# Kernel tuning notes

Measured on AMD Instinct MI355X. Metric: run time of the kernel, lower is better.

## Reference

```python
import jax, jax.numpy as jnp
import numpy as np

EPS = 1e-5  # torch BatchNorm2d default eps (eval mode with running stats)


def bn(x, g, b, m, v):
    # x: [B,C,H,W]; per-channel affine batchnorm in inference form
    return (x - m[:, None, None]) * (g[:, None, None] / jnp.sqrt(v[:, None, None] + EPS)) + b[:, None, None]


def self_attn(x, Wq, bq, Wk, bk, Wv, bv, rel_h, rel_w):
    # x: [B,C,H,W]; Wq/Wk/Wv: [C,C] (1x1 convs); rel_h: [C,H]; rel_w: [C,W]
    B, C, H, W = x.shape
    N = H * W
    q = jnp.einsum('oc,bchw->bohw', Wq, x).reshape(B, C, N) + bq[None, :, None]
    k = jnp.einsum('oc,bchw->bohw', Wk, x).reshape(B, C, N) + bk[None, :, None]
    v = jnp.einsum('oc,bchw->bohw', Wv, x).reshape(B, C, N) + bv[None, :, None]
    energy = jnp.einsum('bcn,bcm->bnm', q, k)                      # content: Q^T K
    pos = (rel_h[:, :, None] + rel_w[:, None, :]).reshape(C, N)    # [C, H*W]
    energy = energy + jnp.einsum('bcn,cm->bnm', q, pos)            # rel-pos bias term
    attn = jax.nn.softmax(energy, axis=-1)                         # [B,N,N]
    out = jnp.einsum('bcm,bnm->bcn', v, attn)                      # V @ attn^T
    return out.reshape(B, C, H, W)


def conv3x3(x, w):
    return jax.lax.conv_general_dilated(x, w, (1, 1), 'SAME',
                                        dimension_numbers=('NCHW', 'OIHW', 'NCHW'))


def setup_inputs() -> dict:
    key = jax.random.key(0)
    B, C, H, W, NH = 32, 512, 16, 16, 5
    ks = jax.random.split(key, 32)
    f = lambda i, shape, s=1.0: jax.random.normal(ks[i], shape, jnp.float32) * s
    inp = {
        'x0': f(0, (B, C, H, W)), 'x1': f(1, (B, C, H, W)), 'x2': f(2, (B, C, H, W)),
        'x3': f(3, (B, C, H, W)), 'x': f(4, (B, C, H, W)),
        'qW': f(5, (NH, C, C), 0.02), 'qB': f(6, (NH, C), 0.02),
        'kW': f(7, (NH, C, C), 0.02), 'kB': f(8, (NH, C), 0.02),
        'vW': f(9, (NH, C, C), 0.02), 'vB': f(10, (NH, C), 0.02),
        'relH': f(11, (NH, C, H)), 'relW': f(12, (NH, C, W)),
        'msw_W': f(13, (NH - 1, NH * C), 0.02),
        'msw_g': jnp.ones((NH - 1,)), 'msw_b': jnp.zeros((NH - 1,)),
        'msw_m': jnp.zeros((NH - 1,)), 'msw_v': jnp.ones((NH - 1,)),
        'fus_W': f(14, (C, C, 3, 3), 0.02),
        'fus_g': jnp.ones((C,)), 'fus_b': jnp.zeros((C,)),
        'fus_m': jnp.zeros((C,)), 'fus_v': jnp.ones((C,)),
        'top_g': jnp.ones((C,)), 'top_b': jnp.zeros((C,)),
        'top_m': jnp.zeros((C,)), 'top_v': jnp.ones((C,)),
        'h': 16, 'w': 16,
    }
    return inp


def reference(x0, x1, x2, x3, x, qW, qB, kW, kB, vW, vB, relH, relW,
              msw_W, msw_g, msw_b, msw_m, msw_v,
              fus_W, fus_g, fus_b, fus_m, fus_v,
              top_g, top_b, top_m, top_v, h, w):
    B, C, H, W = x.shape
    xs = jnp.stack([x0, x1, x2, x3, x])                            # [5,B,C,H,W]
    outs = jax.vmap(self_attn)(xs, qW, qB, kW, kB, vW, vB, relH, relW)  # [5,B,C,H,W]
    cat = outs.transpose(1, 0, 2, 3, 4).reshape(B, 5 * C, H, W)
    weights = jax.nn.sigmoid(bn(jnp.einsum('oc,bchw->bohw', msw_W, cat),
                                msw_g, msw_b, msw_m, msw_v))        # [B,4,H,W]
    x_ms = (weights[:, 0:1] * outs[0] + weights[:, 1:2] * outs[1]
            + weights[:, 2:3] * outs[2] + weights[:, 3:4] * outs[3] + outs[4])
    x_ms = jax.nn.relu(bn(conv3x3(x_ms, fus_W), fus_g, fus_b, fus_m, fus_v))
    out = jax.nn.relu(bn(x_ms + x, top_g, top_b, top_m, top_v))
    return out
```

## Files before the change

### kernel.cpp

```cpp
#include <hip/hip_runtime.h>
#include <cstdint>

using bf16x8  = __attribute__((ext_vector_type(8))) __bf16;
using f32x4   = __attribute__((ext_vector_type(4))) float;
using ushort8 = __attribute__((ext_vector_type(8))) unsigned short;

#define EPSN 1e-5f

__device__ __forceinline__ void gld16(const void* g, void* l) {
  __builtin_amdgcn_global_load_lds((const __attribute__((address_space(1))) void*)g,
                                   (__attribute__((address_space(3))) void*)l, 16, 0, 0);
}

__device__ __forceinline__ ushort f2bf(float f) {
  union { float f; uint32_t u; } v; v.f = f;
  uint32_t r = v.u + 0x7fffu + ((v.u >> 16) & 1u);
  return (ushort)(r >> 16);
}
__device__ __forceinline__ float bf2f(ushort u) {
  union { uint32_t u; float f; } v; v.u = ((uint32_t)u) << 16; return v.f;
}

__device__ __forceinline__ void gemm_core(const ushort* __restrict__ Ag,
                                          const ushort* __restrict__ Bg,
                                          int ldk, int ksteps,
                                          ushort* As, ushort* Bs,
                                          f32x4 (&acc)[4][4]) {
  const int t = threadIdx.x, lane = t & 63, w = t >> 6;
  const int wr = w >> 1, wc = w & 1;
  for (int kt = 0; kt < ksteps; ++kt) {
    const int kbase = kt * 64;
#pragma unroll
    for (int p = 0; p < 4; ++p) {
      int q = p * 256 + t;
      int row = q >> 3, slot = q & 7;
      int srcs = slot ^ (row & 7);
      gld16(Ag + (size_t)row * ldk + kbase + srcs * 8, As + (p * 256 + w * 64) * 8);
      gld16(Bg + (size_t)row * ldk + kbase + srcs * 8, Bs + (p * 256 + w * 64) * 8);
    }
    __syncthreads();
#pragma unroll
    for (int kk = 0; kk < 2; ++kk) {
      bf16x8 af[4], bfv[4];
#pragma unroll
      for (int i = 0; i < 4; ++i) {
        int ra = wr * 64 + i * 16 + (lane & 15);
        int sa = (kk * 4 + (lane >> 4)) ^ (ra & 7);
        af[i] = *(const bf16x8*)(As + ra * 64 + sa * 8);
        int rb = wc * 64 + i * 16 + (lane & 15);
        int sb = (kk * 4 + (lane >> 4)) ^ (rb & 7);
        bfv[i] = *(const bf16x8*)(Bs + rb * 64 + sb * 8);
      }
#pragma unroll
      for (int i = 0; i < 4; ++i)
#pragma unroll
        for (int j = 0; j < 4; ++j)
          acc[i][j] = __builtin_amdgcn_mfma_f32_16x16x32_bf16(af[i], bfv[j], acc[i][j], 0, 0, 0);
    }
    __syncthreads();
  }
}

__global__ __launch_bounds__(256) void k_cvtW(const float* __restrict__ qW,
                                              const float* __restrict__ kW,
                                              const float* __restrict__ vW,
                                              ushort* __restrict__ Wb) {
  int idx = blockIdx.x * 256 + threadIdx.x;
  int gi = idx * 4;
  int sel = gi / 1310720;
  int off = gi - sel * 1310720;
  const float* src = sel == 0 ? qW : (sel == 1 ? kW : vW);
  float4 vv = *(const float4*)(src + off);
  int h = off / 262144, rest = off - h * 262144;
  ushort4 o;
  o.x = f2bf(vv.x); o.y = f2bf(vv.y); o.z = f2bf(vv.z); o.w = f2bf(vv.w);
  *(ushort4*)(Wb + (size_t)(h * 3 + sel) * 262144 + rest) = o;
}

__global__ __launch_bounds__(256) void k_cvtWconv(const float* __restrict__ fusW,
                                                  ushort* __restrict__ Wconv) {
  int p = blockIdx.x * 256 + threadIdx.x;
  const float* src = fusW + (size_t)p * 9;
  float vv[9];
#pragma unroll
  for (int s = 0; s < 9; ++s) vv[s] = src[s];
#pragma unroll
  for (int s = 0; s < 9; ++s) Wconv[(size_t)s * 262144 + p] = f2bf(vv[s]);
}

__global__ __launch_bounds__(256) void k_pos(const float* __restrict__ relH,
                                             const float* __restrict__ relW,
                                             ushort* __restrict__ posb) {
  int idx = blockIdx.x * 256 + threadIdx.x;
  int c = idx & 511, m = (idx >> 9) & 255, h = idx >> 17;
  posb[idx] = f2bf(relH[((size_t)h * 512 + c) * 16 + (m >> 4)] +
                   relW[((size_t)h * 512 + c) * 16 + (m & 15)]);
}

__global__ __launch_bounds__(256) void k_transx(const float* __restrict__ x0,
                                                const float* __restrict__ x1,
                                                const float* __restrict__ x2,
                                                const float* __restrict__ x3,
                                                const float* __restrict__ x4,
                                                ushort* __restrict__ xT) {
  int bid = blockIdx.x;
  const int nt4 = bid & 3;  bid >>= 2;
  const int ct  = bid & 7;  bid >>= 3;
  const int b   = bid & 31; bid >>= 5;
  const int ix  = bid;
  const float* xs = ix == 0 ? x0 : ix == 1 ? x1 : ix == 2 ? x2 : ix == 3 ? x3 : x4;
  const float* src = xs + ((size_t)b * 512 + ct * 64) * 256 + nt4 * 64;
  __shared__ float tile[64][65];
  const int t = threadIdx.x;
  const int col = t & 63, rq = t >> 6;
#pragma unroll
  for (int rr = 0; rr < 16; ++rr) {
    int row = rr * 4 + rq;
    tile[row][col] = src[(size_t)row * 256 + col];
  }
  __syncthreads();
  ushort* dst = xT + ((size_t)(ix * 32 + b) * 256 + nt4 * 64) * 512 + ct * 64;
#pragma unroll
  for (int rr = 0; rr < 16; ++rr) {
    int nrow = rr * 4 + rq;
    dst[(size_t)nrow * 512 + col] = f2bf(tile[col][nrow]);
  }
}

__global__ __launch_bounds__(256) void k_qkv(const ushort* __restrict__ Wb,
                                             const ushort* __restrict__ xT,
                                             const ushort* __restrict__ posb,
                                             const float* __restrict__ qB,
                                             const float* __restrict__ kB,
                                             const float* __restrict__ vB,
                                             ushort* __restrict__ qT,
                                             ushort* __restrict__ kpT,
                                             ushort* __restrict__ vv) {
  __shared__ ushort lds[128 * 144];
  ushort* As = lds;
  ushort* Bs = lds + 8192;
  int bid = blockIdx.x;
  bid = (bid & 7) * 480 + (bid >> 3);
  const int h = bid / 768;
  const int r = bid % 768;
  const int t = threadIdx.x, lane = t & 63, w = t >> 6;
  const int wr = w >> 1, wc = w & 1, g = lane >> 4, l = lane & 15;

  f32x4 acc[4][4];
#pragma unroll
  for (int i = 0; i < 4; ++i)
#pragma unroll
    for (int j = 0; j < 4; ++j) acc[i][j] = f32x4{0.f, 0.f, 0.f, 0.f};

  if (r < 512) {
    const int pt = r >> 3, ot = r & 7;
    const bool isq = ot < 4;
    const ushort* Ag = xT + ((size_t)h * 8192 + pt * 128) * 512;
    const ushort* Bg = Wb + ((size_t)(h * 3 + (isq ? 0 : 1)) * 512 + (ot & 3) * 128) * 512;
    gemm_core(Ag, Bg, 512, 8, As, Bs, acc);

    const float* bias = (isq ? qB : kB) + h * 512 + (ot & 3) * 128;
    float bj[4];
#pragma unroll
    for (int j = 0; j < 4; ++j) bj[j] = bias[wc * 64 + j * 16 + l];
    ushort(*Cs)[144] = (ushort(*)[144])lds;
#pragma unroll
    for (int i = 0; i < 4; ++i)
#pragma unroll
      for (int j = 0; j < 4; ++j)
#pragma unroll
        for (int rr = 0; rr < 4; ++rr)
          Cs[wr * 64 + i * 16 + g * 4 + rr][wc * 64 + j * 16 + l] = f2bf(acc[i][j][rr] + bj[j]);
    __syncthreads();
    ushort* dst = isq ? qT : kpT;
#pragma unroll
    for (int it = 0; it < 8; ++it) {
      int lin = it * 256 + t;
      int row = lin >> 4, cc = (lin & 15) * 8;
      int pglob = pt * 128 + row;
      ushort8 cv = *(const ushort8*)&Cs[row][cc];
      if (!isq) {
        ushort8 pv = *(const ushort8*)(posb + ((size_t)h * 256 + (pglob & 255)) * 512 +
                                       (ot & 3) * 128 + cc);
#pragma unroll
        for (int e = 0; e < 8; ++e) cv[e] = f2bf(bf2f(cv[e]) + bf2f(pv[e]));
      }
      *(ushort8*)(dst + ((size_t)h * 8192 + pglob) * 512 + (ot & 3) * 128 + cc) = cv;
    }
  } else {
    const int r2 = r - 512;
    const int mt = r2 >> 6, ntp = r2 & 63;
    const ushort* Ag = Wb + ((size_t)(h * 3 + 2) * 512 + mt * 128) * 512;
    const ushort* Bg = xT + ((size_t)h * 8192 + ntp * 128) * 512;
    gemm_core(Ag, Bg, 512, 8, As, Bs, acc);

    const float* biasv = vB + h * 512 + mt * 128;
    ushort(*Cs)[144] = (ushort(*)[144])lds;
#pragma unroll
    for (int i = 0; i < 4; ++i)
#pragma unroll
      for (int rr = 0; rr < 4; ++rr) {
        int oloc = wr * 64 + i * 16 + g * 4 + rr;
        float bv = biasv[oloc];
#pragma unroll
        for (int j = 0; j < 4; ++j)
          Cs[oloc][wc * 64 + j * 16 + l] = f2bf(acc[i][j][rr] + bv);
      }
    __syncthreads();
    const int b = ntp >> 1, nb = (ntp & 1) * 128;
#pragma unroll
    for (int it = 0; it < 8; ++it) {
      int lin = it * 256 + t;
      int row = lin >> 4, cc = (lin & 15) * 8;
      ushort8 cv = *(const ushort8*)&Cs[row][cc];
      *(ushort8*)(vv + (((size_t)(h * 32 + b)) * 512 + mt * 128 + row) * 256 + nb + cc) = cv;
    }
  }
}

__global__ __launch_bounds__(256) void k_attn(const ushort* __restrict__ qT,
                                              const ushort* __restrict__ kpT,
                                              ushort* __restrict__ attn) {
  __shared__ ushort As[64 * 64];
  __shared__ ushort Bs[256 * 64];
  __shared__ float red[4][64];
  __shared__ float comb[64];
  int bid = blockIdx.x;
  bid = (bid & 7) * 80 + (bid >> 3);
  const int rt = bid & 3;
  const int hb = bid >> 2;
  const ushort* Ag = qT + ((size_t)hb * 256 + rt * 64) * 512;
  const ushort* Bg = kpT + (size_t)hb * 256 * 512;
  const int t = threadIdx.x, lane = t & 63, w = t >> 6, g = lane >> 4, l = lane & 15;

  f32x4 acc[4][4];
#pragma unroll
  for (int i = 0; i < 4; ++i)
#pragma unroll
    for (int j = 0; j < 4; ++j) acc[i][j] = f32x4{0.f, 0.f, 0.f, 0.f};

  for (int kt = 0; kt < 8; ++kt) {
    const int kbase = kt * 64;
#pragma unroll
    for (int p = 0; p < 2; ++p) {
      int q = p * 256 + t;
      int row = q >> 3, slot = q & 7, srcs = slot ^ (row & 7);
      gld16(Ag + (size_t)row * 512 + kbase + srcs * 8, As + (p * 256 + w * 64) * 8);
    }
#pragma unroll
    for (int p = 0; p < 8; ++p) {
      int q = p * 256 + t;
      int row = q >> 3, slot = q & 7, srcs = slot ^ (row & 7);
      gld16(Bg + (size_t)row * 512 + kbase + srcs * 8, Bs + (p * 256 + w * 64) * 8);
    }
    __syncthreads();
#pragma unroll
    for (int kk = 0; kk < 2; ++kk) {
      bf16x8 af[4], bfv[4];
#pragma unroll
      for (int i = 0; i < 4; ++i) {
        int ra = i * 16 + l;
        int sa = (kk * 4 + g) ^ (ra & 7);
        af[i] = *(const bf16x8*)(As + ra * 64 + sa * 8);
        int rb = w * 64 + i * 16 + l;
        int sb = (kk * 4 + g) ^ (rb & 7);
        bfv[i] = *(const bf16x8*)(Bs + rb * 64 + sb * 8);
      }
#pragma unroll
      for (int i = 0; i < 4; ++i)
#pragma unroll
        for (int j = 0; j < 4; ++j)
          acc[i][j] = __builtin_amdgcn_mfma_f32_16x16x32_bf16(af[i], bfv[j], acc[i][j], 0, 0, 0);
    }
    __syncthreads();
  }

#pragma unroll
  for (int i = 0; i < 4; ++i)
#pragma unroll
    for (int rr = 0; rr < 4; ++rr) {
      float v = fmaxf(fmaxf(acc[i][0][rr], acc[i][1][rr]), fmaxf(acc[i][2][rr], acc[i][3][rr]));
#pragma unroll
      for (int m = 1; m < 16; m <<= 1) v = fmaxf(v, __shfl_xor(v, m));
      if (l == 0) red[w][i * 16 + g * 4 + rr] = v;
    }
  __syncthreads();
  if (t < 64) comb[t] = fmaxf(fmaxf(red[0][t], red[1][t]), fmaxf(red[2][t], red[3][t]));
  __syncthreads();
#pragma unroll
  for (int i = 0; i < 4; ++i)
#pragma unroll
    for (int rr = 0; rr < 4; ++rr) {
      float mx = comb[i * 16 + g * 4 + rr];
      float s = 0.f;
#pragma unroll
      for (int j = 0; j < 4; ++j) {
        float e = expf(acc[i][j][rr] - mx);
        acc[i][j][rr] = e;
        s += e;
      }
#pragma unroll
      for (int m = 1; m < 16; m <<= 1) s += __shfl_xor(s, m);
      if (l == 0) red[w][i * 16 + g * 4 + rr] = s;
    }
  __syncthreads();
  if (t < 64) comb[t] = red[0][t] + red[1][t] + red[2][t] + red[3][t];
  __syncthreads();
  ushort* Arow = attn + (size_t)hb * 65536 + (size_t)rt * 64 * 256;
#pragma unroll
  for (int i = 0; i < 4; ++i)
#pragma unroll
    for (int rr = 0; rr < 4; ++rr) {
      int row = i * 16 + g * 4 + rr;
      float inv = 1.f / comb[row];
#pragma unroll
      for (int j = 0; j < 4; ++j)
        Arow[(size_t)row * 256 + w * 64 + j * 16 + l] = f2bf(acc[i][j][rr] * inv);
    }
}

__global__ __launch_bounds__(256) void k_pv(const ushort* __restrict__ attn,
                                            const ushort* __restrict__ vv,
                                            ushort* __restrict__ OT) {
  __shared__ ushort lds[128 * 144];
  ushort* As = lds;
  ushort* Bs = lds + 8192;
  int bid = blockIdx.x;
  bid = (bid & 7) * 160 + (bid >> 3);
  const int nt = bid & 3; bid >>= 2;
  const int mt = bid & 1; bid >>= 1;
  const size_t hb = (size_t)bid;
  const ushort* Ag = attn + (hb * 256 + mt * 128) * 256;
  const ushort* Bg = vv + (hb * 512 + nt * 128) * 256;
  f32x4 acc[4][4];
#pragma unroll
  for (int i = 0; i < 4; ++i)
#pragma unroll
    for (int j = 0; j < 4; ++j) acc[i][j] = f32x4{0.f, 0.f, 0.f, 0.f};
  gemm_core(Ag, Bg, 256, 4, As, Bs, acc);
  const int t = threadIdx.x, lane = t & 63, w = t >> 6;
  const int wr = w >> 1, wc = w & 1, g = lane >> 4, l = lane & 15;
  ushort(*Cs)[144] = (ushort(*)[144])lds;
#pragma unroll
  for (int i = 0; i < 4; ++i)
#pragma unroll
    for (int j = 0; j < 4; ++j)
#pragma unroll
      for (int rr = 0; rr < 4; ++rr)
        Cs[wr * 64 + i * 16 + g * 4 + rr][wc * 64 + j * 16 + l] = f2bf(acc[i][j][rr]);
  __syncthreads();
#pragma unroll
  for (int it = 0; it < 8; ++it) {
    int lin = it * 256 + t;
    int row = lin >> 4, cc = (lin & 15) * 8;
    ushort8 cv = *(const ushort8*)&Cs[row][cc];
    *(ushort8*)(OT + (hb * 256 + mt * 128 + row) * 512 + nt * 128 + cc) = cv;
  }
}

__global__ __launch_bounds__(256) void k_weights(const ushort* __restrict__ OT,
                                                 const float* __restrict__ mswW,
                                                 const float* __restrict__ mg,
                                                 const float* __restrict__ mb,
                                                 const float* __restrict__ mm,
                                                 const float* __restrict__ mv,
                                                 ushort* __restrict__ xmsT) {
  __shared__ float Os[2560];
  __shared__ float part[4][4];
  __shared__ float wsh[4];
  const int t = threadIdx.x, lane = t & 63, w = t >> 6;
  const size_t pix = blockIdx.x;
  for (int h = 0; h < 5; ++h)
    for (int c = t; c < 512; c += 256)
      Os[h * 512 + c] = bf2f(OT[((size_t)h * 8192 + pix) * 512 + c]);
  __syncthreads();
  float a0 = 0.f, a1 = 0.f, a2 = 0.f, a3 = 0.f;
  for (int i = t; i < 2560; i += 256) {
    float o = Os[i];
    a0 += mswW[i] * o;
    a1 += mswW[2560 + i] * o;
    a2 += mswW[5120 + i] * o;
    a3 += mswW[7680 + i] * o;
  }
#pragma unroll
  for (int m = 1; m < 64; m <<= 1) {
    a0 += __shfl_xor(a0, m); a1 += __shfl_xor(a1, m);
    a2 += __shfl_xor(a2, m); a3 += __shfl_xor(a3, m);
  }
  if (lane == 0) { part[w][0] = a0; part[w][1] = a1; part[w][2] = a2; part[w][3] = a3; }
  __syncthreads();
  if (t < 4) {
    float dot = part[0][t] + part[1][t] + part[2][t] + part[3][t];
    float val = (dot - mm[t]) * (mg[t] * rsqrtf(mv[t] + EPSN)) + mb[t];
    wsh[t] = 1.f / (1.f + expf(-val));
  }
  __syncthreads();
  for (int c = t; c < 512; c += 256) {
    float val = wsh[0] * Os[c] + wsh[1] * Os[512 + c] + wsh[2] * Os[1024 + c] +
                wsh[3] * Os[1536 + c] + Os[2048 + c];
    xmsT[pix * 512 + c] = f2bf(val);
  }
}

__global__ __launch_bounds__(256) void k_conv(const ushort* __restrict__ Wconv,
                                              const ushort* __restrict__ xmsT,
                                              float* __restrict__ y1a,
                                              float* __restrict__ y1b) {
  __shared__ ushort As[128 * 64];
  __shared__ ushort xp[180 * 72];
  int bid = blockIdx.x;
  bid = (bid & 7) * 64 + (bid >> 3);
  const int ntl = bid & 1; bid >>= 1;
  const int mt = bid & 3;  bid >>= 2;
  const int halfk = bid & 1; bid >>= 1;
  const int bb = bid;
  const int y0 = ntl * 8;
  const int t = threadIdx.x, lane = t & 63, w = t >> 6, wr = w >> 1, wc = w & 1;
  f32x4 acc[4][4];
#pragma unroll
  for (int i = 0; i < 4; ++i)
#pragma unroll
    for (int j = 0; j < 4; ++j) acc[i][j] = f32x4{0.f, 0.f, 0.f, 0.f};

  for (int cb = halfk * 4; cb < halfk * 4 + 4; ++cb) {
    __syncthreads();
    for (int u = t; u < 1440; u += 256) {
      int slot = u & 7;
      int xpi = (u >> 3) % 18;
      int rl = u / 144;
      int yg = y0 - 1 + rl, xg = xpi - 1;
      uint4 val = make_uint4(0, 0, 0, 0);
      if (yg >= 0 && yg < 16 && (unsigned)xg < 16u)
        val = *(const uint4*)(xmsT + ((size_t)bb * 256 + yg * 16 + xg) * 512 + cb * 64 + slot * 8);
      *(uint4*)(xp + (rl * 18 + xpi) * 72 + slot * 8) = val;
    }
    for (int s = 0; s < 9; ++s) {
#pragma unroll
      for (int p = 0; p < 4; ++p) {
        int q = p * 256 + t;
        int row = q >> 3, slot = q & 7, srcs = slot ^ (row & 7);
        gld16(Wconv + ((size_t)s * 512 + mt * 128 + row) * 512 + cb * 64 + srcs * 8,
              As + (p * 256 + w * 64) * 8);
      }
      __syncthreads();
      const int dy = s / 3, dx = s - dy * 3;
#pragma unroll
      for (int kk = 0; kk < 2; ++kk) {
        bf16x8 af[4], bfv[4];
#pragma unroll
        for (int i = 0; i < 4; ++i) {
          int ra = wr * 64 + i * 16 + (lane & 15);
          int sa = (kk * 4 + (lane >> 4)) ^ (ra & 7);
          af[i] = *(const bf16x8*)(As + ra * 64 + sa * 8);
          int nl = wc * 64 + i * 16 + (lane & 15);
          int pp = ((nl >> 4) + dy) * 18 + (nl & 15) + dx;
          bfv[i] = *(const bf16x8*)(xp + pp * 72 + (kk * 4 + (lane >> 4)) * 8);
        }
#pragma unroll
        for (int i = 0; i < 4; ++i)
#pragma unroll
          for (int j = 0; j < 4; ++j)
            acc[i][j] = __builtin_amdgcn_mfma_f32_16x16x32_bf16(af[i], bfv[j], acc[i][j], 0, 0, 0);
      }
      __syncthreads();
    }
  }
  float* yp = halfk ? y1b : y1a;
  const int o0 = mt * 128 + wr * 64 + ((lane >> 4) << 2);
  const int n0 = ntl * 128 + wc * 64 + (lane & 15);
#pragma unroll
  for (int i = 0; i < 4; ++i)
#pragma unroll
    for (int j = 0; j < 4; ++j)
#pragma unroll
      for (int rr = 0; rr < 4; ++rr) {
        int o = o0 + i * 16 + rr, n = n0 + j * 16;
        yp[((size_t)bb * 512 + o) * 256 + n] = acc[i][j][rr];
      }
}

__global__ __launch_bounds__(256) void k_top(const float* __restrict__ y1a,
                                             const float* __restrict__ y1b,
                                             const float* __restrict__ x,
                                             const float* __restrict__ fg,
                                             const float* __restrict__ fb,
                                             const float* __restrict__ fm,
                                             const float* __restrict__ fv,
                                             const float* __restrict__ tg,
                                             const float* __restrict__ tb,
                                             const float* __restrict__ tm,
                                             const float* __restrict__ tv,
                                             float* __restrict__ out) {
  size_t i4 = ((size_t)blockIdx.x * 256 + threadIdx.x) * 4;
  int c = (int)((i4 >> 8) & 511);
  float4 a = *(const float4*)(y1a + i4);
  float4 bq = *(const float4*)(y1b + i4);
  float4 xx = *(const float4*)(x + i4);
  float sf = fg[c] * rsqrtf(fv[c] + EPSN), mf = fm[c], bf_ = fb[c];
  float st = tg[c] * rsqrtf(tv[c] + EPSN), mt_ = tm[c], bt_ = tb[c];
  float4 o;
  float v;
  v = fmaxf((a.x + bq.x - mf) * sf + bf_, 0.f); o.x = fmaxf((v + xx.x - mt_) * st + bt_, 0.f);
  v = fmaxf((a.y + bq.y - mf) * sf + bf_, 0.f); o.y = fmaxf((v + xx.y - mt_) * st + bt_, 0.f);
  v = fmaxf((a.z + bq.z - mf) * sf + bf_, 0.f); o.z = fmaxf((v + xx.z - mt_) * st + bt_, 0.f);
  v = fmaxf((a.w + bq.w - mf) * sf + bf_, 0.f); o.w = fmaxf((v + xx.w - mt_) * st + bt_, 0.f);
  *(float4*)(out + i4) = o;
}

extern "C" void kernel_launch(void* const* d_in, const int* in_sizes, int n_in,
                              void* d_out, int out_size, void* d_ws, size_t ws_size,
                              hipStream_t stream) {
  const float* x0   = (const float*)d_in[0];
  const float* x1   = (const float*)d_in[1];
  const float* x2   = (const float*)d_in[2];
  const float* x3   = (const float*)d_in[3];
  const float* x4   = (const float*)d_in[4];
  const float* qW   = (const float*)d_in[5];
  const float* qB   = (const float*)d_in[6];
  const float* kW   = (const float*)d_in[7];
  const float* kB   = (const float*)d_in[8];
  const float* vW   = (const float*)d_in[9];
  const float* vB   = (const float*)d_in[10];
  const float* relH = (const float*)d_in[11];
  const float* relW = (const float*)d_in[12];
  const float* mswW = (const float*)d_in[13];
  const float* msg  = (const float*)d_in[14];
  const float* msb  = (const float*)d_in[15];
  const float* msm  = (const float*)d_in[16];
  const float* msv  = (const float*)d_in[17];
  const float* fusW = (const float*)d_in[18];
  const float* fg   = (const float*)d_in[19];
  const float* fb   = (const float*)d_in[20];
  const float* fm   = (const float*)d_in[21];
  const float* fv   = (const float*)d_in[22];
  const float* tg   = (const float*)d_in[23];
  const float* tb   = (const float*)d_in[24];
  const float* tm   = (const float*)d_in[25];
  const float* tv   = (const float*)d_in[26];

  if (ws_size < 180355072ull) return;
  char* ws = (char*)d_ws;
  ushort* xT    = (ushort*)(ws + 0);
  ushort* attn  = (ushort*)(ws + 0);
  ushort* Wconv = (ushort*)(ws + 20971520);
  ushort* qT    = (ushort*)(ws + 41943040);
  ushort* xmsT  = (ushort*)(ws + 41943040);
  float*  y1a   = (float*)(ws + 50331648);
  float*  y1b   = (float*)(ws + 67108864);
  ushort* kpT   = (ushort*)(ws + 83886080);
  ushort* OT    = (ushort*)(ws + 83886080);
  ushort* vv    = (ushort*)(ws + 125829120);
  ushort* Wb    = (ushort*)(ws + 167772160);
  ushort* posb  = (ushort*)(ws + 175636480);

  k_cvtW   <<<3840, 256, 0, stream>>>(qW, kW, vW, Wb);
  k_pos    <<<2560, 256, 0, stream>>>(relH, relW, posb);
  k_transx <<<5120, 256, 0, stream>>>(x0, x1, x2, x3, x4, xT);
  k_qkv    <<<3840, 256, 0, stream>>>(Wb, xT, posb, qB, kB, vB, qT, kpT, vv);
  k_cvtWconv<<<1024, 256, 0, stream>>>(fusW, Wconv);
  k_attn   <<<640,  256, 0, stream>>>(qT, kpT, attn);
  k_pv     <<<1280, 256, 0, stream>>>(attn, vv, OT);
  k_weights<<<8192, 256, 0, stream>>>(OT, mswW, msg, msb, msm, msv, xmsT);
  k_conv   <<<512,  256, 0, stream>>>(Wconv, xmsT, y1a, y1b);
  k_top    <<<4096, 256, 0, stream>>>(y1a, y1b, x4, fg, fb, fm, fv, tg, tb, tm, tv, (float*)d_out);
}
```

Before: 300.8 us.

## Merge prep kernels, stage attention output via LDS, batch conv weight loads

Three preprocessing kernels (x transpose, QKV weight convert, pos bias) merge into one launch, and the conv-weight conversion moves into extra blocks of the attention kernel, reducing the number of launches. The attention kernel stages the softmax output in LDS and writes it out as 16-byte vectors instead of scattered 2-byte stores. k_weights now processes one pixel per wave with vectorized loads and the mixing weights cached in LDS. k_conv loads three taps per barrier to cut synchronisation. LDS row pitches are padded from 144/72 to 148/76 to reduce bank conflicts, and f2bf uses the native bf16 conversion. The extra LDS in k_conv may lower occupancy.

```diff
diff --git a/kernel.cpp b/kernel.cpp
--- a/kernel.cpp
+++ b/kernel.cpp
@@ -13,9 +13,8 @@
 }
 
 __device__ __forceinline__ ushort f2bf(float f) {
-  union { float f; uint32_t u; } v; v.f = f;
-  uint32_t r = v.u + 0x7fffu + ((v.u >> 16) & 1u);
-  return (ushort)(r >> 16);
+  __bf16 h = (__bf16)f;
+  return __builtin_bit_cast(unsigned short, h);
 }
 __device__ __forceinline__ float bf2f(ushort u) {
   union { uint32_t u; float f; } v; v.u = ((uint32_t)u) << 16; return v.f;
@@ -61,69 +60,65 @@
   }
 }
 
-__global__ __launch_bounds__(256) void k_cvtW(const float* __restrict__ qW,
-                                              const float* __restrict__ kW,
-                                              const float* __restrict__ vW,
-                                              ushort* __restrict__ Wb) {
-  int idx = blockIdx.x * 256 + threadIdx.x;
-  int gi = idx * 4;
-  int sel = gi / 1310720;
-  int off = gi - sel * 1310720;
-  const float* src = sel == 0 ? qW : (sel == 1 ? kW : vW);
-  float4 vv = *(const float4*)(src + off);
-  int h = off / 262144, rest = off - h * 262144;
-  ushort4 o;
-  o.x = f2bf(vv.x); o.y = f2bf(vv.y); o.z = f2bf(vv.z); o.w = f2bf(vv.w);
-  *(ushort4*)(Wb + (size_t)(h * 3 + sel) * 262144 + rest) = o;
-}
-
-__global__ __launch_bounds__(256) void k_cvtWconv(const float* __restrict__ fusW,
-                                                  ushort* __restrict__ Wconv) {
-  int p = blockIdx.x * 256 + threadIdx.x;
-  const float* src = fusW + (size_t)p * 9;
-  float vv[9];
-#pragma unroll
-  for (int s = 0; s < 9; ++s) vv[s] = src[s];
-#pragma unroll
-  for (int s = 0; s < 9; ++s) Wconv[(size_t)s * 262144 + p] = f2bf(vv[s]);
-}
-
-__global__ __launch_bounds__(256) void k_pos(const float* __restrict__ relH,
+__global__ __launch_bounds__(256) void k_pre(const float* __restrict__ x0,
+                                             const float* __restrict__ x1,
+                                             const float* __restrict__ x2,
+                                             const float* __restrict__ x3,
+                                             const float* __restrict__ x4,
+                                             const float* __restrict__ qW,
+                                             const float* __restrict__ kW,
+                                             const float* __restrict__ vW,
+                                             const float* __restrict__ relH,
                                              const float* __restrict__ relW,
+                                             ushort* __restrict__ xT,
+                                             ushort* __restrict__ Wb,
                                              ushort* __restrict__ posb) {
-  int idx = blockIdx.x * 256 + threadIdx.x;
-  int c = idx & 511, m = (idx >> 9) & 255, h = idx >> 17;
-  posb[idx] = f2bf(relH[((size_t)h * 512 + c) * 16 + (m >> 4)] +
-                   relW[((size_t)h * 512 + c) * 16 + (m & 15)]);
-}
-
-__global__ __launch_bounds__(256) void k_transx(const float* __restrict__ x0,
-                                                const float* __restrict__ x1,
-                                                const float* __restrict__ x2,
-                                                const float* __restrict__ x3,
-                                                const float* __restrict__ x4,
-                                                ushort* __restrict__ xT) {
+  __shared__ float tile[64][65];
   int bid = blockIdx.x;
-  const int nt4 = bid & 3;  bid >>= 2;
-  const int ct  = bid & 7;  bid >>= 3;
-  const int b   = bid & 31; bid >>= 5;
-  const int ix  = bid;
-  const float* xs = ix == 0 ? x0 : ix == 1 ? x1 : ix == 2 ? x2 : ix == 3 ? x3 : x4;
-  const float* src = xs + ((size_t)b * 512 + ct * 64) * 256 + nt4 * 64;
-  __shared__ float tile[64][65];
   const int t = threadIdx.x;
-  const int col = t & 63, rq = t >> 6;
-#pragma unroll
-  for (int rr = 0; rr < 16; ++rr) {
-    int row = rr * 4 + rq;
-    tile[row][col] = src[(size_t)row * 256 + col];
-  }
-  __syncthreads();
-  ushort* dst = xT + ((size_t)(ix * 32 + b) * 256 + nt4 * 64) * 512 + ct * 64;
-#pragma unroll
-  for (int rr = 0; rr < 16; ++rr) {
-    int nrow = rr * 4 + rq;
-    dst[(size_t)nrow * 512 + col] = f2bf(tile[col][nrow]);
+  if (bid < 5120) {
+    const int nt4 = bid & 3;  bid >>= 2;
+    const int ct  = bid & 7;  bid >>= 3;
+    const int b   = bid & 31; bid >>= 5;
+    const int ix  = bid;
+    const float* xs = ix == 0 ? x0 : ix == 1 ? x1 : ix == 2 ? x2 : ix == 3 ? x3 : x4;
+    const float* src = xs + ((size_t)b * 512 + ct * 64) * 256 + nt4 * 64;
+    const int col = t & 63, rq = t >> 6;
+#pragma unroll
+    for (int rr = 0; rr < 16; ++rr) {
+      int row = rr * 4 + rq;
+      tile[row][col] = src[(size_t)row * 256 + col];
+    }
+    __syncthreads();
+    ushort* dst = xT + ((size_t)(ix * 32 + b) * 256 + nt4 * 64) * 512 + ct * 64;
+#pragma unroll
+    for (int rr = 0; rr < 16; ++rr) {
+      int nrow = rr * 4 + rq;
+      dst[(size_t)nrow * 512 + col] = f2bf(tile[col][nrow]);
+    }
+  } else if (bid < 8960) {
+    int idx = (bid - 5120) * 256 + t;
+    int gi = idx * 4;
+    int sel = gi / 1310720;
+    int off = gi - sel * 1310720;
+    const float* src = sel == 0 ? qW : (sel == 1 ? kW : vW);
+    float4 vv = *(const float4*)(src + off);
+    int h = off / 262144, rest = off - h * 262144;
+    ushort4 o;
+    o.x = f2bf(vv.x); o.y = f2bf(vv.y); o.z = f2bf(vv.z); o.w = f2bf(vv.w);
+    *(ushort4*)(Wb + (size_t)(h * 3 + sel) * 262144 + rest) = o;
+  } else {
+    int idx8 = (bid - 8960) * 256 + t;
+    int e0 = idx8 * 8;
+    int c0 = e0 & 511, m = (e0 >> 9) & 255, h = e0 >> 17;
+    ushort8 o;
+#pragma unroll
+    for (int e = 0; e < 8; ++e) {
+      int c = c0 + e;
+      o[e] = f2bf(relH[((size_t)h * 512 + c) * 16 + (m >> 4)] +
+                  relW[((size_t)h * 512 + c) * 16 + (m & 15)]);
+    }
+    *(ushort8*)(posb + e0) = o;
   }
 }
 
@@ -136,7 +131,7 @@
                                              ushort* __restrict__ qT,
                                              ushort* __restrict__ kpT,
                                              ushort* __restrict__ vv) {
-  __shared__ ushort lds[128 * 144];
+  __shared__ ushort lds[128 * 148];
   ushort* As = lds;
   ushort* Bs = lds + 8192;
   int bid = blockIdx.x;
@@ -163,7 +158,7 @@
     float bj[4];
 #pragma unroll
     for (int j = 0; j < 4; ++j) bj[j] = bias[wc * 64 + j * 16 + l];
-    ushort(*Cs)[144] = (ushort(*)[144])lds;
+    ushort(*Cs)[148] = (ushort(*)[148])lds;
 #pragma unroll
     for (int i = 0; i < 4; ++i)
 #pragma unroll
@@ -195,7 +190,7 @@
     gemm_core(Ag, Bg, 512, 8, As, Bs, acc);
 
     const float* biasv = vB + h * 512 + mt * 128;
-    ushort(*Cs)[144] = (ushort(*)[144])lds;
+    ushort(*Cs)[148] = (ushort(*)[148])lds;
 #pragma unroll
     for (int i = 0; i < 4; ++i)
 #pragma unroll
@@ -220,18 +215,32 @@
 
 __global__ __launch_bounds__(256) void k_attn(const ushort* __restrict__ qT,
                                               const ushort* __restrict__ kpT,
-                                              ushort* __restrict__ attn) {
-  __shared__ ushort As[64 * 64];
-  __shared__ ushort Bs[256 * 64];
+                                              const float* __restrict__ fusW,
+                                              ushort* __restrict__ attn,
+                                              ushort* __restrict__ Wconv) {
+  __shared__ ushort sm[20480];
   __shared__ float red[4][64];
   __shared__ float comb[64];
   int bid = blockIdx.x;
+  const int t = threadIdx.x;
+  if (bid >= 640) {
+    int p = (bid - 640) * 256 + t;
+    const float* src = fusW + (size_t)p * 9;
+    float vv[9];
+#pragma unroll
+    for (int s = 0; s < 9; ++s) vv[s] = src[s];
+#pragma unroll
+    for (int s = 0; s < 9; ++s) Wconv[(size_t)s * 262144 + p] = f2bf(vv[s]);
+    return;
+  }
   bid = (bid & 7) * 80 + (bid >> 3);
   const int rt = bid & 3;
   const int hb = bid >> 2;
+  ushort* As = sm;
+  ushort* Bs = sm + 4096;
   const ushort* Ag = qT + ((size_t)hb * 256 + rt * 64) * 512;
   const ushort* Bg = kpT + (size_t)hb * 256 * 512;
-  const int t = threadIdx.x, lane = t & 63, w = t >> 6, g = lane >> 4, l = lane & 15;
+  const int lane = t & 63, w = t >> 6, g = lane >> 4, l = lane & 15;
 
   f32x4 acc[4][4];
 #pragma unroll
@@ -306,7 +315,7 @@
   __syncthreads();
   if (t < 64) comb[t] = red[0][t] + red[1][t] + red[2][t] + red[3][t];
   __syncthreads();
-  ushort* Arow = attn + (size_t)hb * 65536 + (size_t)rt * 64 * 256;
+  ushort(*P)[260] = (ushort(*)[260])sm;
 #pragma unroll
   for (int i = 0; i < 4; ++i)
 #pragma unroll
@@ -315,14 +324,23 @@
       float inv = 1.f / comb[row];
 #pragma unroll
       for (int j = 0; j < 4; ++j)
-        Arow[(size_t)row * 256 + w * 64 + j * 16 + l] = f2bf(acc[i][j][rr] * inv);
-    }
+        P[row][w * 64 + j * 16 + l] = f2bf(acc[i][j][rr] * inv);
+    }
+  __syncthreads();
+  ushort* Arow = attn + (size_t)hb * 65536 + (size_t)rt * 16384;
+#pragma unroll
+  for (int it = 0; it < 8; ++it) {
+    int lin = it * 256 + t;
+    int row = lin >> 5, c8 = (lin & 31) * 8;
+    ushort8 cv = *(const ushort8*)&P[row][c8];
+    *(ushort8*)(Arow + (size_t)row * 256 + c8) = cv;
+  }
 }
 
 __global__ __launch_bounds__(256) void k_pv(const ushort* __restrict__ attn,
                                             const ushort* __restrict__ vv,
                                             ushort* __restrict__ OT) {
-  __shared__ ushort lds[128 * 144];
+  __shared__ ushort lds[128 * 148];
   ushort* As = lds;
   ushort* Bs = lds + 8192;
   int bid = blockIdx.x;
@@ -340,7 +358,7 @@
   gemm_core(Ag, Bg, 256, 4, As, Bs, acc);
   const int t = threadIdx.x, lane = t & 63, w = t >> 6;
   const int wr = w >> 1, wc = w & 1, g = lane >> 4, l = lane & 15;
-  ushort(*Cs)[144] = (ushort(*)[144])lds;
+  ushort(*Cs)[148] = (ushort(*)[148])lds;
 #pragma unroll
   for (int i = 0; i < 4; ++i)
 #pragma unroll
@@ -365,49 +383,66 @@
                                                  const float* __restrict__ mm,
                                                  const float* __restrict__ mv,
                                                  ushort* __restrict__ xmsT) {
-  __shared__ float Os[2560];
-  __shared__ float part[4][4];
-  __shared__ float wsh[4];
+  __shared__ float msw[10240];
   const int t = threadIdx.x, lane = t & 63, w = t >> 6;
-  const size_t pix = blockIdx.x;
+#pragma unroll
+  for (int it = 0; it < 10; ++it) {
+    int idx = it * 1024 + t * 4;
+    *(float4*)(msw + idx) = *(const float4*)(mswW + idx);
+  }
+  __syncthreads();
+  const size_t pix = (size_t)blockIdx.x * 4 + w;
+  float o[5][2][4];
+#pragma unroll
   for (int h = 0; h < 5; ++h)
-    for (int c = t; c < 512; c += 256)
-      Os[h * 512 + c] = bf2f(OT[((size_t)h * 8192 + pix) * 512 + c]);
-  __syncthreads();
-  float a0 = 0.f, a1 = 0.f, a2 = 0.f, a3 = 0.f;
-  for (int i = t; i < 2560; i += 256) {
-    float o = Os[i];
-    a0 += mswW[i] * o;
-    a1 += mswW[2560 + i] * o;
-    a2 += mswW[5120 + i] * o;
-    a3 += mswW[7680 + i] * o;
-  }
+#pragma unroll
+    for (int hf = 0; hf < 2; ++hf) {
+      ushort4 v = *(const ushort4*)(OT + ((size_t)h * 8192 + pix) * 512 + hf * 256 + lane * 4);
+      o[h][hf][0] = bf2f(v.x); o[h][hf][1] = bf2f(v.y);
+      o[h][hf][2] = bf2f(v.z); o[h][hf][3] = bf2f(v.w);
+    }
+  float a[4] = {0.f, 0.f, 0.f, 0.f};
+#pragma unroll
+  for (int j = 0; j < 4; ++j)
+#pragma unroll
+    for (int h = 0; h < 5; ++h)
+#pragma unroll
+      for (int hf = 0; hf < 2; ++hf) {
+        float4 m4 = *(const float4*)(msw + j * 2560 + h * 512 + hf * 256 + lane * 4);
+        a[j] += m4.x * o[h][hf][0] + m4.y * o[h][hf][1] +
+                m4.z * o[h][hf][2] + m4.w * o[h][hf][3];
+      }
 #pragma unroll
   for (int m = 1; m < 64; m <<= 1) {
-    a0 += __shfl_xor(a0, m); a1 += __shfl_xor(a1, m);
-    a2 += __shfl_xor(a2, m); a3 += __shfl_xor(a3, m);
-  }
-  if (lane == 0) { part[w][0] = a0; part[w][1] = a1; part[w][2] = a2; part[w][3] = a3; }
-  __syncthreads();
-  if (t < 4) {
-    float dot = part[0][t] + part[1][t] + part[2][t] + part[3][t];
-    float val = (dot - mm[t]) * (mg[t] * rsqrtf(mv[t] + EPSN)) + mb[t];
-    wsh[t] = 1.f / (1.f + expf(-val));
-  }
-  __syncthreads();
-  for (int c = t; c < 512; c += 256) {
-    float val = wsh[0] * Os[c] + wsh[1] * Os[512 + c] + wsh[2] * Os[1024 + c] +
-                wsh[3] * Os[1536 + c] + Os[2048 + c];
-    xmsT[pix * 512 + c] = f2bf(val);
-  }
+    a[0] += __shfl_xor(a[0], m); a[1] += __shfl_xor(a[1], m);
+    a[2] += __shfl_xor(a[2], m); a[3] += __shfl_xor(a[3], m);
+  }
+  float wj[4];
+#pragma unroll
+  for (int j = 0; j < 4; ++j) {
+    float val = (a[j] - mm[j]) * (mg[j] * rsqrtf(mv[j] + EPSN)) + mb[j];
+    wj[j] = 1.f / (1.f + expf(-val));
+  }
+#pragma unroll
+  for (int hf = 0; hf < 2; ++hf) {
+    ushort4 ov;
+    float* op = (float*)&ov;
+    float r0 = wj[0] * o[0][hf][0] + wj[1] * o[1][hf][0] + wj[2] * o[2][hf][0] + wj[3] * o[3][hf][0] + o[4][hf][0];
+    float r1 = wj[0] * o[0][hf][1] + wj[1] * o[1][hf][1] + wj[2] * o[2][hf][1] + wj[3] * o[3][hf][1] + o[4][hf][1];
+    float r2 = wj[0] * o[0][hf][2] + wj[1] * o[1][hf][2] + wj[2] * o[2][hf][2] + wj[3] * o[3][hf][2] + o[4][hf][2];
+    float r3 = wj[0] * o[0][hf][3] + wj[1] * o[1][hf][3] + wj[2] * o[2][hf][3] + wj[3] * o[3][hf][3] + o[4][hf][3];
+    ushort4 pk; pk.x = f2bf(r0); pk.y = f2bf(r1); pk.z = f2bf(r2); pk.w = f2bf(r3);
+    *(ushort4*)(xmsT + pix * 512 + hf * 256 + lane * 4) = pk;
+  }
+  (void)0;
 }
 
 __global__ __launch_bounds__(256) void k_conv(const ushort* __restrict__ Wconv,
                                               const ushort* __restrict__ xmsT,
                                               float* __restrict__ y1a,
                                               float* __restrict__ y1b) {
-  __shared__ ushort As[128 * 64];
-  __shared__ ushort xp[180 * 72];
+  __shared__ ushort As3[3 * 128 * 64];
+  __shared__ ushort xp[180 * 76];
   int bid = blockIdx.x;
   bid = (bid & 7) * 64 + (bid >> 3);
   const int ntl = bid & 1; bid >>= 1;
@@ -432,36 +467,39 @@
       uint4 val = make_uint4(0, 0, 0, 0);
       if (yg >= 0 && yg < 16 && (unsigned)xg < 16u)
         val = *(const uint4*)(xmsT + ((size_t)bb * 256 + yg * 16 + xg) * 512 + cb * 64 + slot * 8);
-      *(uint4*)(xp + (rl * 18 + xpi) * 72 + slot * 8) = val;
-    }
-    for (int s = 0; s < 9; ++s) {
-#pragma unroll
-      for (int p = 0; p < 4; ++p) {
-        int q = p * 256 + t;
-        int row = q >> 3, slot = q & 7, srcs = slot ^ (row & 7);
-        gld16(Wconv + ((size_t)s * 512 + mt * 128 + row) * 512 + cb * 64 + srcs * 8,
-              As + (p * 256 + w * 64) * 8);
-      }
+      *(uint4*)(xp + (rl * 18 + xpi) * 76 + slot * 8) = val;
+    }
+    for (int dy = 0; dy < 3; ++dy) {
+#pragma unroll
+      for (int dx = 0; dx < 3; ++dx)
+#pragma unroll
+        for (int p = 0; p < 4; ++p) {
+          int q = p * 256 + t;
+          int row = q >> 3, slot = q & 7, srcs = slot ^ (row & 7);
+          gld16(Wconv + ((size_t)(dy * 3 + dx) * 512 + mt * 128 + row) * 512 + cb * 64 + srcs * 8,
+                As3 + dx * 8192 + (p * 256 + w * 64) * 8);
+        }
       __syncthreads();
-      const int dy = s / 3, dx = s - dy * 3;
-#pragma unroll
-      for (int kk = 0; kk < 2; ++kk) {
-        bf16x8 af[4], bfv[4];
-#pragma unroll
-        for (int i = 0; i < 4; ++i) {
-          int ra = wr * 64 + i * 16 + (lane & 15);
-          int sa = (kk * 4 + (lane >> 4)) ^ (ra & 7);
-          af[i] = *(const bf16x8*)(As + ra * 64 + sa * 8);
-          int nl = wc * 64 + i * 16 + (lane & 15);
-          int pp = ((nl >> 4) + dy) * 18 + (nl & 15) + dx;
-          bfv[i] = *(const bf16x8*)(xp + pp * 72 + (kk * 4 + (lane >> 4)) * 8);
+#pragma unroll
+      for (int dx = 0; dx < 3; ++dx)
+#pragma unroll
+        for (int kk = 0; kk < 2; ++kk) {
+          bf16x8 af[4], bfv[4];
+#pragma unroll
+          for (int i = 0; i < 4; ++i) {
+            int ra = wr * 64 + i * 16 + (lane & 15);
+            int sa = (kk * 4 + (lane >> 4)) ^ (ra & 7);
+            af[i] = *(const bf16x8*)(As3 + dx * 8192 + ra * 64 + sa * 8);
+            int nl = wc * 64 + i * 16 + (lane & 15);
+            int pp = ((nl >> 4) + dy) * 18 + (nl & 15) + dx;
+            bfv[i] = *(const bf16x8*)(xp + pp * 76 + (kk * 4 + (lane >> 4)) * 8);
+          }
+#pragma unroll
+          for (int i = 0; i < 4; ++i)
+#pragma unroll
+            for (int j = 0; j < 4; ++j)
+              acc[i][j] = __builtin_amdgcn_mfma_f32_16x16x32_bf16(af[i], bfv[j], acc[i][j], 0, 0, 0);
         }
-#pragma unroll
-        for (int i = 0; i < 4; ++i)
-#pragma unroll
-          for (int j = 0; j < 4; ++j)
-            acc[i][j] = __builtin_amdgcn_mfma_f32_16x16x32_bf16(af[i], bfv[j], acc[i][j], 0, 0, 0);
-      }
       __syncthreads();
     }
   }
@@ -553,14 +591,12 @@
   ushort* Wb    = (ushort*)(ws + 167772160);
   ushort* posb  = (ushort*)(ws + 175636480);
 
-  k_cvtW   <<<3840, 256, 0, stream>>>(qW, kW, vW, Wb);
-  k_pos    <<<2560, 256, 0, stream>>>(relH, relW, posb);
-  k_transx <<<5120, 256, 0, stream>>>(x0, x1, x2, x3, x4, xT);
+  k_pre    <<<9280, 256, 0, stream>>>(x0, x1, x2, x3, x4, qW, kW, vW, relH, relW,
+                                      xT, Wb, posb);
   k_qkv    <<<3840, 256, 0, stream>>>(Wb, xT, posb, qB, kB, vB, qT, kpT, vv);
-  k_cvtWconv<<<1024, 256, 0, stream>>>(fusW, Wconv);
-  k_attn   <<<640,  256, 0, stream>>>(qT, kpT, attn);
+  k_attn   <<<1664, 256, 0, stream>>>(qT, kpT, fusW, attn, Wconv);
   k_pv     <<<1280, 256, 0, stream>>>(attn, vv, OT);
-  k_weights<<<8192, 256, 0, stream>>>(OT, mswW, msg, msb, msm, msv, xmsT);
+  k_weights<<<2048, 256, 0, stream>>>(OT, mswW, msg, msb, msm, msv, xmsT);
   k_conv   <<<512,  256, 0, stream>>>(Wconv, xmsT, y1a, y1b);
   k_top    <<<4096, 256, 0, stream>>>(y1a, y1b, x4, fg, fb, fm, fv, tg, tb, tm, tv, (float*)d_out);
 }
```

After: 272.2 us. 1.11x faster.
